# Kernel optimization log

Hardware: AMD Instinct MI355X
Metric: run time of the kernel (lower is better)

The kernel has to match this reference:

```python
import jax, jax.numpy as jnp
import numpy as np

B, OUT, EXC_IN, INH_IN, BF = 8192, 1024, 4096, 2048, 4
K_EXC, K_INH = 32, 16


def _pruned_weight(pre_w, K):
    # TopKLinear.pruned_weight: mask of top-K entries (by pre_w) times exp(pre_w)
    w = jnp.exp(pre_w)                      # param_space='log'
    _, idx = jax.lax.top_k(pre_w, K)        # [out, K] indices per row
    rows = jnp.arange(pre_w.shape[0])[:, None]
    mask = jnp.zeros_like(pre_w).at[rows, idx].set(1.0)
    return mask * w


def setup_inputs() -> dict:
    key = jax.random.key(0)
    ks = jax.random.split(key, 5)
    return {
        "x": jax.random.normal(ks[0], (B, EXC_IN), jnp.float32),
        "inhibitory_input": jax.random.normal(ks[1], (B, INH_IN), jnp.float32),
        "branch_input": jax.random.normal(ks[2], (B, OUT * BF), jnp.float32),
        "pre_w_exc": jax.random.uniform(ks[3], (OUT, EXC_IN), jnp.float32, -2.1, -2.0),
        "pre_w_inh": jax.random.uniform(ks[4], (OUT, INH_IN), jnp.float32, -2.1, -2.0),
        "w_block": jnp.ones((OUT, BF), jnp.float32),          # BlockLinear weight (init ones, frozen)
        "presigmoid_Vth": jnp.full((OUT,), -2.0, jnp.float32),  # uniform(-2,-2) == constant
        "log_alpha_max": jnp.zeros((OUT,), jnp.float32),
    }


def reference(x, inhibitory_input, branch_input, pre_w_exc, pre_w_inh,
              w_block, presigmoid_Vth, log_alpha_max):
    # TopKLinear forward: x @ pruned_weight.T
    excitation = x @ _pruned_weight(pre_w_exc, K_EXC).T            # [B, OUT]
    inhibition = inhibitory_input @ _pruned_weight(pre_w_inh, K_INH).T  # [B, OUT]

    # BlockLinear: scatter w_block into block-diagonal [OUT, OUT*BF] then mm;
    # equivalent contraction over the block dim only.
    current = jnp.einsum('nob,ob->no', branch_input.reshape(B, OUT, BF), w_block)
    conductance = jnp.sum(w_block, axis=1)                         # [OUT]

    numerator = excitation + current
    denominator = excitation + 1.0 + conductance + inhibition
    voltage = numerator / denominator

    # reactivation
    Vth = jax.nn.sigmoid(presigmoid_Vth)
    V_diff = voltage - Vth
    rate = jnp.exp(log_alpha_max) * V_diff * V_diff
    return jnp.where(V_diff < 0, jnp.zeros((), voltage.dtype), rate)
```

## Files before the change

kernel.cpp:

```cpp
#include <hip/hip_runtime.h>
#include <cstdint>
#include <cstddef>

#define B_ROWS 8192
#define OUT_N  1024
#define EXC_IN 4096
#define INH_IN 2048
#define K_EXC  32
#define K_INH  16
#define TILE_N 4

template<int COLS, int K>
__device__ __forceinline__ void topk_row(const float* __restrict__ src,
                                         float2* __restrict__ orow, int lane)
{
    constexpr int E4 = COLS / 256;
    unsigned long long keys[E4 * 4];
#pragma unroll
    for (int i = 0; i < E4; ++i) {
        const float4 v = ((const float4*)src)[i * 64 + lane];
        const float vv[4] = {v.x, v.y, v.z, v.w};
#pragma unroll
        for (int q = 0; q < 4; ++q) {
            const int idx = (i * 64 + lane) * 4 + q;
            const unsigned int u = __float_as_uint(vv[q]);
            const unsigned int m = (u >> 31) ? ~u : (u | 0x80000000u);
            keys[i * 4 + q] = ((unsigned long long)m << 12)
                            | (unsigned long long)(4095 - idx);
        }
    }

    unsigned long long win = 0xFFFFFFFFFFFFFFFFull;
#pragma unroll 1
    for (int r = 0; r < K; ++r) {
        unsigned long long best = 0ull;
#pragma unroll
        for (int i = 0; i < E4 * 4; ++i) {
            const unsigned long long k2 = (keys[i] == win) ? 0ull : keys[i];
            keys[i] = k2;
            best = (k2 > best) ? k2 : best;
        }
#pragma unroll
        for (int m = 1; m < 64; m <<= 1) {
            const unsigned long long o = __shfl_xor(best, m, 64);
            best = (o > best) ? o : best;
        }
        win = best;
        if (lane == 0) {
            const unsigned int idx = 4095u - (unsigned int)(win & 0xFFFull);
            const unsigned int mm  = (unsigned int)(win >> 12);
            const unsigned int u   = (mm & 0x80000000u) ? (mm & 0x7FFFFFFFu) : ~mm;
            const float v = __uint_as_float(u);
            orow[r] = make_float2(expf(v), __uint_as_float(idx));
        }
    }
}

__global__ __launch_bounds__(256, 1) void topk_both_kernel(
    const float* __restrict__ pwe, const float* __restrict__ pwi,
    float2* __restrict__ wexc, float2* __restrict__ winh)
{
    const int wid  = (blockIdx.x * 256 + threadIdx.x) >> 6;
    const int lane = threadIdx.x & 63;
    if (wid < OUT_N) {
        topk_row<EXC_IN, K_EXC>(pwe + (size_t)wid * EXC_IN,
                                wexc + (size_t)wid * K_EXC, lane);
    } else {
        const int r = wid - OUT_N;
        topk_row<INH_IN, K_INH>(pwi + (size_t)r * INH_IN,
                                winh + (size_t)r * K_INH, lane);
    }
}

__device__ __forceinline__ float4 xpose4(float4 v, int j)
{
    const float u0 = __shfl_xor(v.y, 1, 64), u1 = __shfl_xor(v.x, 1, 64);
    const float u2 = __shfl_xor(v.w, 1, 64), u3 = __shfl_xor(v.z, 1, 64);
    if (j & 1) { v.x = u0; v.z = u2; } else { v.y = u1; v.w = u3; }
    const float w0 = __shfl_xor(v.z, 2, 64), w1 = __shfl_xor(v.w, 2, 64);
    const float w2 = __shfl_xor(v.x, 2, 64), w3 = __shfl_xor(v.y, 2, 64);
    if (j & 2) { v.x = w0; v.y = w1; } else { v.z = w2; v.w = w3; }
    return v;
}

__global__ __launch_bounds__(256, 2) void dendritic_main_kernel(
    const float*  __restrict__ x,
    const float*  __restrict__ inh,
    const float4* __restrict__ branch,
    const float2* __restrict__ wexc,
    const float2* __restrict__ winh,
    const float4* __restrict__ wblock,
    const float*  __restrict__ presig,
    const float*  __restrict__ logalpha,
    float*        __restrict__ out)
{
    __shared__ float sx[EXC_IN * TILE_N];

    const int tid = threadIdx.x;
    const int n0  = blockIdx.x * TILE_N;
    const int jq  = tid & 3;
    const int c4b = tid >> 2;

#pragma unroll
    for (int it = 0; it < (EXC_IN * TILE_N / 4) / 256; ++it) {
        const int c4 = c4b + it * 64;
        float4 v = ((const float4*)(x + (size_t)(n0 + jq) * EXC_IN))[c4];
        v = xpose4(v, jq);
        ((float4*)sx)[it * 256 + tid] = v;
    }
    __syncthreads();

    float acc_e[4][TILE_N];
#pragma unroll
    for (int j = 0; j < 4; ++j)
#pragma unroll
        for (int n = 0; n < TILE_N; ++n) acc_e[j][n] = 0.f;

#pragma unroll
    for (int j = 0; j < 4; ++j) {
        const int o = tid + j * 256;
        const float2* wr = wexc + (size_t)o * K_EXC;
#pragma unroll 8
        for (int k = 0; k < K_EXC; ++k) {
            const float2 wv = wr[k];
            const int c = (int)__float_as_uint(wv.y);
            const float4 xv = ((const float4*)sx)[c];
            acc_e[j][0] = fmaf(xv.x, wv.x, acc_e[j][0]);
            acc_e[j][1] = fmaf(xv.y, wv.x, acc_e[j][1]);
            acc_e[j][2] = fmaf(xv.z, wv.x, acc_e[j][2]);
            acc_e[j][3] = fmaf(xv.w, wv.x, acc_e[j][3]);
        }
    }
    __syncthreads();

#pragma unroll
    for (int it = 0; it < (INH_IN * TILE_N / 4) / 256; ++it) {
        const int c4 = c4b + it * 64;
        float4 v = ((const float4*)(inh + (size_t)(n0 + jq) * INH_IN))[c4];
        v = xpose4(v, jq);
        ((float4*)sx)[it * 256 + tid] = v;
    }
    __syncthreads();

    float acc_i[4][TILE_N];
#pragma unroll
    for (int j = 0; j < 4; ++j)
#pragma unroll
        for (int n = 0; n < TILE_N; ++n) acc_i[j][n] = 0.f;

#pragma unroll
    for (int j = 0; j < 4; ++j) {
        const int o = tid + j * 256;
        const float2* wr = winh + (size_t)o * K_INH;
#pragma unroll 8
        for (int k = 0; k < K_INH; ++k) {
            const float2 wv = wr[k];
            const int c = (int)__float_as_uint(wv.y);
            const float4 xv = ((const float4*)sx)[c];
            acc_i[j][0] = fmaf(xv.x, wv.x, acc_i[j][0]);
            acc_i[j][1] = fmaf(xv.y, wv.x, acc_i[j][1]);
            acc_i[j][2] = fmaf(xv.z, wv.x, acc_i[j][2]);
            acc_i[j][3] = fmaf(xv.w, wv.x, acc_i[j][3]);
        }
    }

#pragma unroll
    for (int j = 0; j < 4; ++j) {
        const int o = tid + j * 256;
        const float4 wb = wblock[o];
        const float cond  = wb.x + wb.y + wb.z + wb.w;
        const float Vth   = 1.f / (1.f + expf(-presig[o]));
        const float alpha = expf(logalpha[o]);
#pragma unroll
        for (int n = 0; n < TILE_N; ++n) {
            const float4 br = branch[(size_t)(n0 + n) * OUT_N + o];
            const float cur = br.x * wb.x + br.y * wb.y + br.z * wb.z + br.w * wb.w;
            const float e  = acc_e[j][n];
            const float ii = acc_i[j][n];
            const float num = e + cur;
            const float den = e + 1.f + cond + ii;
            const float v   = num / den;
            const float d   = v - Vth;
            const float r   = alpha * d * d;
            out[(size_t)(n0 + n) * OUT_N + o] = (d < 0.f) ? 0.f : r;
        }
    }
}

extern "C" void kernel_launch(void* const* d_in, const int* in_sizes, int n_in,
                              void* d_out, int out_size, void* d_ws, size_t ws_size,
                              hipStream_t stream)
{
    const float* x      = (const float*)d_in[0];
    const float* inh    = (const float*)d_in[1];
    const float* branch = (const float*)d_in[2];
    const float* pwe    = (const float*)d_in[3];
    const float* pwi    = (const float*)d_in[4];
    const float* wb     = (const float*)d_in[5];
    const float* ps     = (const float*)d_in[6];
    const float* la     = (const float*)d_in[7];
    float* out = (float*)d_out;

    float2* wexc = (float2*)d_ws;
    float2* winh = (float2*)((char*)d_ws + (size_t)OUT_N * K_EXC * sizeof(float2));

    topk_both_kernel<<<(2 * OUT_N) / 4, 256, 0, stream>>>(pwe, pwi, wexc, winh);

    dendritic_main_kernel<<<B_ROWS / TILE_N, 256, 0, stream>>>(
        x, inh, (const float4*)branch, wexc, winh,
        (const float4*)wb, ps, la, out);
}
```

Measured before the change: 458.7 us.

## Stage x/inh tiles via direct global-to-LDS loads and prefetch branch input early

Replaces the register load plus shuffle-transpose staging of x and inhibitory rows with direct global_load_lds transfers that write the transposed layout straight into shared memory. Branch inputs are loaded into registers before the first barrier so their latency overlaps the staging and sparse matmul. The block grows to 512 threads with two outputs per thread, and weight/index pairs are read as float4 to halve load instructions. Occupancy hints change and register pressure rises from holding the prefetched branch data.

Result: slower. 482.7 us (+5.2%).

```diff
diff --git a/kernel.cpp b/kernel.cpp
--- a/kernel.cpp
+++ b/kernel.cpp
@@ -9,6 +9,7 @@
 #define K_EXC  32
 #define K_INH  16
 #define TILE_N 4
+#define MAIN_THREADS 512
 
 template<int COLS, int K>
 __device__ __forceinline__ void topk_row(const float* __restrict__ src,
@@ -72,18 +73,10 @@
     }
 }
 
-__device__ __forceinline__ float4 xpose4(float4 v, int j)
-{
-    const float u0 = __shfl_xor(v.y, 1, 64), u1 = __shfl_xor(v.x, 1, 64);
-    const float u2 = __shfl_xor(v.w, 1, 64), u3 = __shfl_xor(v.z, 1, 64);
-    if (j & 1) { v.x = u0; v.z = u2; } else { v.y = u1; v.w = u3; }
-    const float w0 = __shfl_xor(v.z, 2, 64), w1 = __shfl_xor(v.w, 2, 64);
-    const float w2 = __shfl_xor(v.x, 2, 64), w3 = __shfl_xor(v.y, 2, 64);
-    if (j & 2) { v.x = w0; v.y = w1; } else { v.z = w2; v.w = w3; }
-    return v;
-}
-
-__global__ __launch_bounds__(256, 2) void dendritic_main_kernel(
+typedef __attribute__((address_space(1))) const unsigned int gu32_t;
+typedef __attribute__((address_space(3))) unsigned int lu32_t;
+
+__global__ __launch_bounds__(MAIN_THREADS, 4) void dendritic_main_kernel(
     const float*  __restrict__ x,
     const float*  __restrict__ inh,
     const float4* __restrict__ branch,
@@ -96,85 +89,109 @@
 {
     __shared__ float sx[EXC_IN * TILE_N];
 
-    const int tid = threadIdx.x;
-    const int n0  = blockIdx.x * TILE_N;
-    const int jq  = tid & 3;
-    const int c4b = tid >> 2;
-
-#pragma unroll
-    for (int it = 0; it < (EXC_IN * TILE_N / 4) / 256; ++it) {
-        const int c4 = c4b + it * 64;
-        float4 v = ((const float4*)(x + (size_t)(n0 + jq) * EXC_IN))[c4];
-        v = xpose4(v, jq);
-        ((float4*)sx)[it * 256 + tid] = v;
-    }
+    const int tid  = threadIdx.x;
+    const int lane = tid & 63;
+    const int wv   = tid >> 6;
+    const int n0   = blockIdx.x * TILE_N;
+
+    const float* xsrc = x + (size_t)(n0 + (lane & 3)) * EXC_IN + (lane >> 2);
+#pragma unroll
+    for (int it = 0; it < 32; ++it) {
+        const int chunk = it * 8 + wv;
+        __builtin_amdgcn_global_load_lds(
+            (gu32_t*)(xsrc + chunk * 16),
+            (lu32_t*)(sx + chunk * 64), 4, 0, 0);
+    }
+
+    float4 br[2][TILE_N];
+#pragma unroll
+    for (int j = 0; j < 2; ++j) {
+        const int o = tid + j * MAIN_THREADS;
+#pragma unroll
+        for (int n = 0; n < TILE_N; ++n)
+            br[j][n] = branch[(size_t)(n0 + n) * OUT_N + o];
+    }
+
     __syncthreads();
 
-    float acc_e[4][TILE_N];
-#pragma unroll
-    for (int j = 0; j < 4; ++j)
+    float acc_e[2][TILE_N];
+#pragma unroll
+    for (int j = 0; j < 2; ++j)
 #pragma unroll
         for (int n = 0; n < TILE_N; ++n) acc_e[j][n] = 0.f;
 
 #pragma unroll
-    for (int j = 0; j < 4; ++j) {
-        const int o = tid + j * 256;
-        const float2* wr = wexc + (size_t)o * K_EXC;
+    for (int j = 0; j < 2; ++j) {
+        const int o = tid + j * MAIN_THREADS;
+        const float4* wr = (const float4*)(wexc + (size_t)o * K_EXC);
 #pragma unroll 8
-        for (int k = 0; k < K_EXC; ++k) {
-            const float2 wv = wr[k];
-            const int c = (int)__float_as_uint(wv.y);
-            const float4 xv = ((const float4*)sx)[c];
-            acc_e[j][0] = fmaf(xv.x, wv.x, acc_e[j][0]);
-            acc_e[j][1] = fmaf(xv.y, wv.x, acc_e[j][1]);
-            acc_e[j][2] = fmaf(xv.z, wv.x, acc_e[j][2]);
-            acc_e[j][3] = fmaf(xv.w, wv.x, acc_e[j][3]);
+        for (int k = 0; k < K_EXC / 2; ++k) {
+            const float4 wv2 = wr[k];
+            const int c0 = (int)__float_as_uint(wv2.y);
+            const int c1 = (int)__float_as_uint(wv2.w);
+            const float4 x0 = ((const float4*)sx)[c0];
+            const float4 x1 = ((const float4*)sx)[c1];
+            acc_e[j][0] = fmaf(x0.x, wv2.x, acc_e[j][0]);
+            acc_e[j][1] = fmaf(x0.y, wv2.x, acc_e[j][1]);
+            acc_e[j][2] = fmaf(x0.z, wv2.x, acc_e[j][2]);
+            acc_e[j][3] = fmaf(x0.w, wv2.x, acc_e[j][3]);
+            acc_e[j][0] = fmaf(x1.x, wv2.z, acc_e[j][0]);
+            acc_e[j][1] = fmaf(x1.y, wv2.z, acc_e[j][1]);
+            acc_e[j][2] = fmaf(x1.z, wv2.z, acc_e[j][2]);
+            acc_e[j][3] = fmaf(x1.w, wv2.z, acc_e[j][3]);
         }
     }
     __syncthreads();
 
-#pragma unroll
-    for (int it = 0; it < (INH_IN * TILE_N / 4) / 256; ++it) {
-        const int c4 = c4b + it * 64;
-        float4 v = ((const float4*)(inh + (size_t)(n0 + jq) * INH_IN))[c4];
-        v = xpose4(v, jq);
-        ((float4*)sx)[it * 256 + tid] = v;
+    const float* isrc = inh + (size_t)(n0 + (lane & 3)) * INH_IN + (lane >> 2);
+#pragma unroll
+    for (int it = 0; it < 16; ++it) {
+        const int chunk = it * 8 + wv;
+        __builtin_amdgcn_global_load_lds(
+            (gu32_t*)(isrc + chunk * 16),
+            (lu32_t*)(sx + chunk * 64), 4, 0, 0);
     }
     __syncthreads();
 
-    float acc_i[4][TILE_N];
-#pragma unroll
-    for (int j = 0; j < 4; ++j)
+    float acc_i[2][TILE_N];
+#pragma unroll
+    for (int j = 0; j < 2; ++j)
 #pragma unroll
         for (int n = 0; n < TILE_N; ++n) acc_i[j][n] = 0.f;
 
 #pragma unroll
-    for (int j = 0; j < 4; ++j) {
-        const int o = tid + j * 256;
-        const float2* wr = winh + (size_t)o * K_INH;
+    for (int j = 0; j < 2; ++j) {
+        const int o = tid + j * MAIN_THREADS;
+        const float4* wr = (const float4*)(winh + (size_t)o * K_INH);
 #pragma unroll 8
-        for (int k = 0; k < K_INH; ++k) {
-            const float2 wv = wr[k];
-            const int c = (int)__float_as_uint(wv.y);
-            const float4 xv = ((const float4*)sx)[c];
-            acc_i[j][0] = fmaf(xv.x, wv.x, acc_i[j][0]);
-            acc_i[j][1] = fmaf(xv.y, wv.x, acc_i[j][1]);
-            acc_i[j][2] = fmaf(xv.z, wv.x, acc_i[j][2]);
-            acc_i[j][3] = fmaf(xv.w, wv.x, acc_i[j][3]);
-        }
-    }
-
-#pragma unroll
-    for (int j = 0; j < 4; ++j) {
-        const int o = tid + j * 256;
+        for (int k = 0; k < K_INH / 2; ++k) {
+            const float4 wv2 = wr[k];
+            const int c0 = (int)__float_as_uint(wv2.y);
+            const int c1 = (int)__float_as_uint(wv2.w);
+            const float4 x0 = ((const float4*)sx)[c0];
+            const float4 x1 = ((const float4*)sx)[c1];
+            acc_i[j][0] = fmaf(x0.x, wv2.x, acc_i[j][0]);
+            acc_i[j][1] = fmaf(x0.y, wv2.x, acc_i[j][1]);
+            acc_i[j][2] = fmaf(x0.z, wv2.x, acc_i[j][2]);
+            acc_i[j][3] = fmaf(x0.w, wv2.x, acc_i[j][3]);
+            acc_i[j][0] = fmaf(x1.x, wv2.z, acc_i[j][0]);
+            acc_i[j][1] = fmaf(x1.y, wv2.z, acc_i[j][1]);
+            acc_i[j][2] = fmaf(x1.z, wv2.z, acc_i[j][2]);
+            acc_i[j][3] = fmaf(x1.w, wv2.z, acc_i[j][3]);
+        }
+    }
+
+#pragma unroll
+    for (int j = 0; j < 2; ++j) {
+        const int o = tid + j * MAIN_THREADS;
         const float4 wb = wblock[o];
         const float cond  = wb.x + wb.y + wb.z + wb.w;
         const float Vth   = 1.f / (1.f + expf(-presig[o]));
         const float alpha = expf(logalpha[o]);
 #pragma unroll
         for (int n = 0; n < TILE_N; ++n) {
-            const float4 br = branch[(size_t)(n0 + n) * OUT_N + o];
-            const float cur = br.x * wb.x + br.y * wb.y + br.z * wb.z + br.w * wb.w;
+            const float4 b4 = br[j][n];
+            const float cur = b4.x * wb.x + b4.y * wb.y + b4.z * wb.z + b4.w * wb.w;
             const float e  = acc_e[j][n];
             const float ii = acc_i[j][n];
             const float num = e + cur;
@@ -206,7 +223,7 @@
 
     topk_both_kernel<<<(2 * OUT_N) / 4, 256, 0, stream>>>(pwe, pwi, wexc, winh);
 
-    dendritic_main_kernel<<<B_ROWS / TILE_N, 256, 0, stream>>>(
+    dendritic_main_kernel<<<B_ROWS / TILE_N, MAIN_THREADS, 0, stream>>>(
         x, inh, (const float4*)branch, wexc, winh,
         (const float4*)wb, ps, la, out);
 }
```

## Persistent 1024-thread main kernel with double-buffered async LDS loads and transposed top-k weights

Applied to the files above, without the earlier changes.

Restructures the main kernel so that 512 persistent blocks of 1024 threads each loop over 2-row tiles. One thread handles each output column. The x and inhibitory rows are prefetched straight into a double-buffered LDS tile with global_load_lds, so the next tile loads while the current one is computed. The top-k weight/index pairs are stored transposed (k-major) so per-thread weight loads coalesce across output columns, and the shuffle transpose is dropped. This adds hand-written vmcnt waits and raw barriers, which depend on the exact count of outstanding loads and could be fragile, and it needs a large LDS footprint (48 KB per buffer pair) with reduced row reuse per tile.

New measurement: 465.7 us. No clear change (+1.5%).

```diff
diff --git a/kernel.cpp b/kernel.cpp
--- a/kernel.cpp
+++ b/kernel.cpp
@@ -8,11 +8,19 @@
 #define INH_IN 2048
 #define K_EXC  32
 #define K_INH  16
-#define TILE_N 4
+
+#define TILE_N       2
+#define MAIN_THREADS 1024
+#define NBLK         512
+#define NT_PER_BLK   (B_ROWS / TILE_N / NBLK)
+#define COMB_FLOATS  ((EXC_IN + INH_IN) * TILE_N)
+#define CHUNKS       (COMB_FLOATS / 64)
+#define CHUNKS_PER_WAVE (CHUNKS / (MAIN_THREADS / 64))
+#define XCHUNKS      (EXC_IN * TILE_N / 64)
 
 template<int COLS, int K>
 __device__ __forceinline__ void topk_row(const float* __restrict__ src,
-                                         float2* __restrict__ orow, int lane)
+                                         float2* __restrict__ ocol, int lane)
 {
     constexpr int E4 = COLS / 256;
     unsigned long long keys[E4 * 4];
@@ -51,139 +59,135 @@
             const unsigned int mm  = (unsigned int)(win >> 12);
             const unsigned int u   = (mm & 0x80000000u) ? (mm & 0x7FFFFFFFu) : ~mm;
             const float v = __uint_as_float(u);
-            orow[r] = make_float2(expf(v), __uint_as_float(idx));
+            ocol[(size_t)r * OUT_N] = make_float2(expf(v), __uint_as_float(idx));
         }
     }
 }
 
 __global__ __launch_bounds__(256, 1) void topk_both_kernel(
     const float* __restrict__ pwe, const float* __restrict__ pwi,
-    float2* __restrict__ wexc, float2* __restrict__ winh)
+    float2* __restrict__ wexcT, float2* __restrict__ winhT)
 {
     const int wid  = (blockIdx.x * 256 + threadIdx.x) >> 6;
     const int lane = threadIdx.x & 63;
     if (wid < OUT_N) {
-        topk_row<EXC_IN, K_EXC>(pwe + (size_t)wid * EXC_IN,
-                                wexc + (size_t)wid * K_EXC, lane);
+        topk_row<EXC_IN, K_EXC>(pwe + (size_t)wid * EXC_IN, wexcT + wid, lane);
     } else {
         const int r = wid - OUT_N;
-        topk_row<INH_IN, K_INH>(pwi + (size_t)r * INH_IN,
-                                winh + (size_t)r * K_INH, lane);
-    }
-}
-
-__device__ __forceinline__ float4 xpose4(float4 v, int j)
-{
-    const float u0 = __shfl_xor(v.y, 1, 64), u1 = __shfl_xor(v.x, 1, 64);
-    const float u2 = __shfl_xor(v.w, 1, 64), u3 = __shfl_xor(v.z, 1, 64);
-    if (j & 1) { v.x = u0; v.z = u2; } else { v.y = u1; v.w = u3; }
-    const float w0 = __shfl_xor(v.z, 2, 64), w1 = __shfl_xor(v.w, 2, 64);
-    const float w2 = __shfl_xor(v.x, 2, 64), w3 = __shfl_xor(v.y, 2, 64);
-    if (j & 2) { v.x = w0; v.y = w1; } else { v.z = w2; v.w = w3; }
-    return v;
-}
-
-__global__ __launch_bounds__(256, 2) void dendritic_main_kernel(
+        topk_row<INH_IN, K_INH>(pwi + (size_t)r * INH_IN, winhT + r, lane);
+    }
+}
+
+typedef __attribute__((address_space(1))) const unsigned int gu32_t;
+typedef __attribute__((address_space(3))) unsigned int lu32_t;
+
+__global__ __launch_bounds__(MAIN_THREADS, 4) void dendritic_main_kernel(
     const float*  __restrict__ x,
     const float*  __restrict__ inh,
     const float4* __restrict__ branch,
-    const float2* __restrict__ wexc,
-    const float2* __restrict__ winh,
+    const float2* __restrict__ wexcT,
+    const float2* __restrict__ winhT,
     const float4* __restrict__ wblock,
     const float*  __restrict__ presig,
     const float*  __restrict__ logalpha,
     float*        __restrict__ out)
 {
-    __shared__ float sx[EXC_IN * TILE_N];
-
-    const int tid = threadIdx.x;
-    const int n0  = blockIdx.x * TILE_N;
-    const int jq  = tid & 3;
-    const int c4b = tid >> 2;
-
-#pragma unroll
-    for (int it = 0; it < (EXC_IN * TILE_N / 4) / 256; ++it) {
-        const int c4 = c4b + it * 64;
-        float4 v = ((const float4*)(x + (size_t)(n0 + jq) * EXC_IN))[c4];
-        v = xpose4(v, jq);
-        ((float4*)sx)[it * 256 + tid] = v;
-    }
-    __syncthreads();
-
-    float acc_e[4][TILE_N];
-#pragma unroll
-    for (int j = 0; j < 4; ++j)
-#pragma unroll
-        for (int n = 0; n < TILE_N; ++n) acc_e[j][n] = 0.f;
-
-#pragma unroll
-    for (int j = 0; j < 4; ++j) {
-        const int o = tid + j * 256;
-        const float2* wr = wexc + (size_t)o * K_EXC;
+    __shared__ float sx[2][COMB_FLOATS];
+
+    const int tid  = threadIdx.x;
+    const int lane = tid & 63;
+    const int w    = tid >> 6;
+    const int o    = tid;
+
+    const float4 wb   = wblock[o];
+    const float cond  = wb.x + wb.y + wb.z + wb.w;
+    const float Vth   = 1.f / (1.f + expf(-presig[o]));
+    const float alpha = expf(logalpha[o]);
+
+    const int tile0 = blockIdx.x * NT_PER_BLK;
+    const int srow  = lane & 1;
+    const int scol  = lane >> 1;
+
+    {
+        const int n0 = tile0 * TILE_N;
+        const float* xs = x   + (size_t)(n0 + srow) * EXC_IN + scol;
+        const float* is = inh + (size_t)(n0 + srow) * INH_IN + scol;
+#pragma unroll
+        for (int i = 0; i < CHUNKS_PER_WAVE; ++i) {
+            const int c = i * 16 + w;
+            const float* src = (c < XCHUNKS) ? (xs + c * 32)
+                                             : (is + (c - XCHUNKS) * 32);
+            __builtin_amdgcn_global_load_lds((gu32_t*)src,
+                                             (lu32_t*)(&sx[0][0] + c * 64),
+                                             4, 0, 0);
+        }
+    }
+
+#pragma unroll 1
+    for (int t = 0; t < NT_PER_BLK; ++t) {
+        const int n0 = (tile0 + t) * TILE_N;
+        const float* buf = &sx[t & 1][0];
+
+        if (t + 1 < NT_PER_BLK) {
+            const int n1 = n0 + TILE_N;
+            const float* xs = x   + (size_t)(n1 + srow) * EXC_IN + scol;
+            const float* is = inh + (size_t)(n1 + srow) * INH_IN + scol;
+            float* dst = &sx[(t + 1) & 1][0];
+#pragma unroll
+            for (int i = 0; i < CHUNKS_PER_WAVE; ++i) {
+                const int c = i * 16 + w;
+                const float* src = (c < XCHUNKS) ? (xs + c * 32)
+                                                 : (is + (c - XCHUNKS) * 32);
+                __builtin_amdgcn_global_load_lds((gu32_t*)src,
+                                                 (lu32_t*)(dst + c * 64),
+                                                 4, 0, 0);
+            }
+        }
+
+        const float4 br0 = branch[(size_t)(n0 + 0) * OUT_N + o];
+        const float4 br1 = branch[(size_t)(n0 + 1) * OUT_N + o];
+
+        if (t + 1 < NT_PER_BLK) {
+            asm volatile("s_waitcnt vmcnt(14)" ::: "memory");
+        } else {
+            asm volatile("s_waitcnt vmcnt(2)" ::: "memory");
+        }
+        __builtin_amdgcn_s_barrier();
+
+        float e0 = 0.f, e1 = 0.f;
 #pragma unroll 8
         for (int k = 0; k < K_EXC; ++k) {
-            const float2 wv = wr[k];
+            const float2 wv = wexcT[k * OUT_N + o];
             const int c = (int)__float_as_uint(wv.y);
-            const float4 xv = ((const float4*)sx)[c];
-            acc_e[j][0] = fmaf(xv.x, wv.x, acc_e[j][0]);
-            acc_e[j][1] = fmaf(xv.y, wv.x, acc_e[j][1]);
-            acc_e[j][2] = fmaf(xv.z, wv.x, acc_e[j][2]);
-            acc_e[j][3] = fmaf(xv.w, wv.x, acc_e[j][3]);
-        }
-    }
-    __syncthreads();
-
-#pragma unroll
-    for (int it = 0; it < (INH_IN * TILE_N / 4) / 256; ++it) {
-        const int c4 = c4b + it * 64;
-        float4 v = ((const float4*)(inh + (size_t)(n0 + jq) * INH_IN))[c4];
-        v = xpose4(v, jq);
-        ((float4*)sx)[it * 256 + tid] = v;
-    }
-    __syncthreads();
-
-    float acc_i[4][TILE_N];
-#pragma unroll
-    for (int j = 0; j < 4; ++j)
-#pragma unroll
-        for (int n = 0; n < TILE_N; ++n) acc_i[j][n] = 0.f;
-
-#pragma unroll
-    for (int j = 0; j < 4; ++j) {
-        const int o = tid + j * 256;
-        const float2* wr = winh + (size_t)o * K_INH;
+            const float2 xv = ((const float2*)buf)[c];
+            e0 = fmaf(xv.x, wv.x, e0);
+            e1 = fmaf(xv.y, wv.x, e1);
+        }
+
+        float i0 = 0.f, i1 = 0.f;
 #pragma unroll 8
         for (int k = 0; k < K_INH; ++k) {
-            const float2 wv = wr[k];
+            const float2 wv = winhT[k * OUT_N + o];
             const int c = (int)__float_as_uint(wv.y);
-            const float4 xv = ((const float4*)sx)[c];
-            acc_i[j][0] = fmaf(xv.x, wv.x, acc_i[j][0]);
-            acc_i[j][1] = fmaf(xv.y, wv.x, acc_i[j][1]);
-            acc_i[j][2] = fmaf(xv.z, wv.x, acc_i[j][2]);
-            acc_i[j][3] = fmaf(xv.w, wv.x, acc_i[j][3]);
-        }
-    }
-
-#pragma unroll
-    for (int j = 0; j < 4; ++j) {
-        const int o = tid + j * 256;
-        const float4 wb = wblock[o];
-        const float cond  = wb.x + wb.y + wb.z + wb.w;
-        const float Vth   = 1.f / (1.f + expf(-presig[o]));
-        const float alpha = expf(logalpha[o]);
-#pragma unroll
-        for (int n = 0; n < TILE_N; ++n) {
-            const float4 br = branch[(size_t)(n0 + n) * OUT_N + o];
-            const float cur = br.x * wb.x + br.y * wb.y + br.z * wb.z + br.w * wb.w;
-            const float e  = acc_e[j][n];
-            const float ii = acc_i[j][n];
-            const float num = e + cur;
-            const float den = e + 1.f + cond + ii;
-            const float v   = num / den;
-            const float d   = v - Vth;
-            const float r   = alpha * d * d;
-            out[(size_t)(n0 + n) * OUT_N + o] = (d < 0.f) ? 0.f : r;
-        }
+            const float2 xv = ((const float2*)buf)[EXC_IN + c];
+            i0 = fmaf(xv.x, wv.x, i0);
+            i1 = fmaf(xv.y, wv.x, i1);
+        }
+
+        {
+            const float cur0 = br0.x * wb.x + br0.y * wb.y + br0.z * wb.z + br0.w * wb.w;
+            const float cur1 = br1.x * wb.x + br1.y * wb.y + br1.z * wb.z + br1.w * wb.w;
+            const float v0 = (e0 + cur0) / (e0 + 1.f + cond + i0);
+            const float v1 = (e1 + cur1) / (e1 + 1.f + cond + i1);
+            const float d0 = v0 - Vth;
+            const float d1 = v1 - Vth;
+            const float r0 = alpha * d0 * d0;
+            const float r1 = alpha * d1 * d1;
+            out[(size_t)(n0 + 0) * OUT_N + o] = (d0 < 0.f) ? 0.f : r0;
+            out[(size_t)(n0 + 1) * OUT_N + o] = (d1 < 0.f) ? 0.f : r1;
+        }
+
+        __builtin_amdgcn_s_barrier();
     }
 }
 
@@ -201,12 +205,12 @@
     const float* la     = (const float*)d_in[7];
     float* out = (float*)d_out;
 
-    float2* wexc = (float2*)d_ws;
-    float2* winh = (float2*)((char*)d_ws + (size_t)OUT_N * K_EXC * sizeof(float2));
-
-    topk_both_kernel<<<(2 * OUT_N) / 4, 256, 0, stream>>>(pwe, pwi, wexc, winh);
-
-    dendritic_main_kernel<<<B_ROWS / TILE_N, 256, 0, stream>>>(
-        x, inh, (const float4*)branch, wexc, winh,
+    float2* wexcT = (float2*)d_ws;
+    float2* winhT = (float2*)((char*)d_ws + (size_t)OUT_N * K_EXC * sizeof(float2));
+
+    topk_both_kernel<<<(2 * OUT_N) / 4, 256, 0, stream>>>(pwe, pwi, wexcT, winhT);
+
+    dendritic_main_kernel<<<NBLK, MAIN_THREADS, 0, stream>>>(
+        x, inh, (const float4*)branch, wexcT, winhT,
         (const float4*)wb, ps, la, out);
 }
```
